# Kernel tuning notes

Measured on AMD Instinct MI355X. Metric: run time of the kernel, lower is better.

Reference implementation:

```python
import jax, jax.numpy as jnp
import numpy as np

N_LAYERS = 2
N_QUBITS = 2


def _ry(t):
    c, s = jnp.cos(t / 2), jnp.sin(t / 2)
    m = jnp.stack([jnp.stack([c, -s], -1), jnp.stack([s, c], -1)], -2)
    return m.astype(jnp.complex64)


def _rx(t):
    c = jnp.cos(t / 2).astype(jnp.complex64)
    s = (-1j) * jnp.sin(t / 2).astype(jnp.complex64)
    return jnp.stack([jnp.stack([c, s], -1), jnp.stack([s, c], -1)], -2)


def _rz(t):
    e = jnp.exp(-0.5j * t.astype(jnp.complex64))
    z = jnp.zeros_like(e)
    return jnp.stack([jnp.stack([e, z], -1), jnp.stack([z, jnp.conj(e)], -1)], -2)


def _apply_w0(G, s):
    # gate on wire 0 (most significant); s: [N,2,2] indexed [n, q0, q1]
    if G.ndim == 2:
        G = G[None]
    return jnp.matmul(G, s)


def _apply_w1(G, s):
    # gate on wire 1: contract last index with G
    if G.ndim == 2:
        G = G[None]
    return jnp.matmul(s, jnp.swapaxes(G, -1, -2))


def _qnn_batched(enc, qw):
    # enc: [N,2] float angles; qw: [2,2,3] trainable angles.
    # Batched 2-qubit statevector simulation, state shape [N,2,2] (q0,q1).
    N = enc.shape[0]
    s = jnp.zeros((N, 2, 2), jnp.complex64).at[:, 0, 0].set(1.0)
    # data encoding: RY(enc_i) on wire i
    s = _apply_w0(_ry(enc[:, 0]), s)
    s = _apply_w1(_ry(enc[:, 1]), s)
    for l in range(N_LAYERS):
        # RX then RY then RZ on each qubit => fused single-qubit gate RZ@RY@RX
        g0 = _rz(qw[l, 0, 2]) @ _ry(qw[l, 0, 1]) @ _rx(qw[l, 0, 0])
        g1 = _rz(qw[l, 1, 2]) @ _ry(qw[l, 1, 1]) @ _rx(qw[l, 1, 0])
        s = _apply_w0(g0, s)
        s = _apply_w1(g1, s)
        # CNOT(control=0, target=1): flip q1 where q0 == 1
        s = s.at[:, 1, :].set(s[:, 1, ::-1])
    p = (s * jnp.conj(s)).real  # probabilities [N,2,2]
    z0 = (p[:, 0, :] - p[:, 1, :]).sum(-1)
    z1 = (p[:, :, 0] - p[:, :, 1]).sum(-1)
    return jnp.stack([z0, z1], -1)  # [N,2]


def _mlp(x, w1, b1, w2, b2, w3, b3):
    h = jnp.tanh(x @ w1 + b1)
    h = jnp.tanh(h @ w2 + b2)
    return h @ w3 + b3


def setup_inputs() -> dict:
    key = jax.random.key(0)
    ks = jax.random.split(key, 15)
    N = 1_000_000
    W = 32

    def rn(k, shape, scale):
        return (scale * jax.random.normal(k, shape)).astype(jnp.float32)

    return {
        "x": rn(ks[0], (N, 1), 1.0),
        "pre_w1": rn(ks[1], (1, W), 1.0),
        "pre_b1": rn(ks[2], (W,), 0.1),
        "pre_w2": rn(ks[3], (W, W), 1.0 / np.sqrt(W)),
        "pre_b2": rn(ks[4], (W,), 0.1),
        "pre_w3": rn(ks[5], (W, 2), 1.0 / np.sqrt(W)),
        "pre_b3": rn(ks[6], (2,), 0.1),
        "q_weights": rn(ks[7], (N_LAYERS, N_QUBITS, 3), 0.1),
        "post_w1": rn(ks[8], (2, W), 1.0 / np.sqrt(2)),
        "post_b1": rn(ks[9], (W,), 0.1),
        "post_w2": rn(ks[10], (W, W), 1.0 / np.sqrt(W)),
        "post_b2": rn(ks[11], (W,), 0.1),
        "post_w3": rn(ks[12], (W, 1), 1.0 / np.sqrt(W)),
        "post_b3": rn(ks[13], (1,), 0.1),
    }


def reference(x, pre_w1, pre_b1, pre_w2, pre_b2, pre_w3, pre_b3, q_weights,
              post_w1, post_b1, post_w2, post_b2, post_w3, post_b3):
    q = _mlp(x, pre_w1, pre_b1, pre_w2, pre_b2, pre_w3, pre_b3)        # [N,2]
    qhat = _qnn_batched(q, q_weights)                                  # [N,2]
    u = _mlp(qhat, post_w1, post_b1, post_w2, post_b2, post_w3, post_b3)  # [N,1]
    return u
```

## Files before the change

### kernel.cpp

```cpp
#include <hip/hip_runtime.h>
#include <hip/hip_bf16.h>
#include <math.h>
#include <stdint.h>


typedef __attribute__((ext_vector_type(8))) short short8;
typedef __attribute__((ext_vector_type(4))) float f32x4;

union Frag { uint32_t u[4]; short8 s; };

#define KT 2.8853900817779268f

#define L_FRAG 0
#define L_U    2048
#define L_W1   2080
#define L_B1   2112
#define L_BH2  2144
#define L_W3   2176
#define L_OW1  2240
#define L_OB1  2304
#define L_BH2P 2336
#define L_OW3  2368
#define L_SC   2400
#define L_TOT  2416

__device__ __forceinline__ float sig_act(float y) {
    return __builtin_amdgcn_rcpf(__builtin_amdgcn_exp2f(y) + 1.0f);
}

__device__ __forceinline__ uint32_t pk_bf16(float a, float b) {
    union { __hip_bfloat162 h; uint32_t u; } cv;
    cv.h.x = __float2bfloat16(a);
    cv.h.y = __float2bfloat16(b);
    return cv.u;
}

__device__ __forceinline__ void split8(const float h[8], uint32_t hi[4], uint32_t lo[4]) {
    #pragma unroll
    for (int p = 0; p < 4; ++p) {
        uint32_t u0 = __float_as_uint(h[2*p])   & 0xFFFF0000u;
        uint32_t u1 = __float_as_uint(h[2*p+1]) & 0xFFFF0000u;
        float l0 = h[2*p]   - __uint_as_float(u0);
        float l1 = h[2*p+1] - __uint_as_float(u1);
        uint32_t v0 = __float_as_uint(l0) & 0xFFFF0000u;
        uint32_t v1 = __float_as_uint(l1) & 0xFFFF0000u;
        hi[p] = (u0 >> 16) | u1;
        lo[p] = (v0 >> 16) | v1;
    }
}

struct cplx { float re, im; };
__device__ __forceinline__ cplx cmul(cplx a, cplx b) {
    return { a.re * b.re - a.im * b.im, a.re * b.im + a.im * b.re };
}
__device__ __forceinline__ cplx cadd(cplx a, cplx b) {
    return { a.re + b.re, a.im + b.im };
}

__global__ void qcpinn_setup(
    const float* __restrict__ pw1, const float* __restrict__ pb1,
    const float* __restrict__ pw2, const float* __restrict__ pb2,
    const float* __restrict__ pw3, const float* __restrict__ pb3,
    const float* __restrict__ qw,
    const float* __restrict__ ow1, const float* __restrict__ ob1,
    const float* __restrict__ ow2, const float* __restrict__ ob2,
    const float* __restrict__ ow3, const float* __restrict__ ob3,
    float* __restrict__ ws)
{
    const int lane = threadIdx.x & 63;
    const int s = lane & 15, gg = lane >> 4;
    uint32_t* wsu = (uint32_t*)ws;

    #pragma unroll
    for (int m = 0; m < 2; ++m) {
        const float* W = m ? ow2 : pw2;
        #pragma unroll
        for (int r = 0; r < 2; ++r) {
            float v[8];
            #pragma unroll
            for (int j = 0; j < 8; ++j)
                v[j] = -2.0f * KT * W[(gg * 8 + j) * 32 + (r * 16 + s)];
            uint32_t hi[4], lo[4];
            split8(v, hi, lo);
            int bh = L_FRAG + ((m * 4 + r * 2 + 0) * 256) + lane * 4;
            int bl = L_FRAG + ((m * 4 + r * 2 + 1) * 256) + lane * 4;
            #pragma unroll
            for (int p = 0; p < 4; ++p) { wsu[bh + p] = hi[p]; wsu[bl + p] = lo[p]; }
        }
    }

    if (lane < 32) {
        int j = lane;
        float cs_p = 0.f, cs_o = 0.f;
        for (int k = 0; k < 32; ++k) { cs_p += pw2[k * 32 + j]; cs_o += ow2[k * 32 + j]; }
        ws[L_W1 + j]   = KT * pw1[j];
        ws[L_B1 + j]   = KT * pb1[j];
        ws[L_BH2 + j]  = KT * (pb2[j] + cs_p);
        ws[L_OB1 + j]  = KT * ob1[j];
        ws[L_BH2P + j] = KT * (ob2[j] + cs_o);
        ws[L_OW3 + j]  = -2.f * ow3[j];
        ws[L_W3 + j * 2]     = -pw3[j * 2];
        ws[L_W3 + j * 2 + 1] = -pw3[j * 2 + 1];
        float sg0 = (j & 16) ? -1.f : 1.f;
        float sg1 = (j & 8)  ? -1.f : 1.f;
        ws[L_OW1 + j]      = KT * sg0 * ow1[j];
        ws[L_OW1 + 32 + j] = KT * sg1 * ow1[32 + j];
    }

    if (lane == 0) {
        float cw0 = 0.f, cw1 = 0.f, co3 = 0.f;
        for (int k = 0; k < 32; ++k) {
            cw0 += pw3[k * 2]; cw1 += pw3[k * 2 + 1]; co3 += ow3[k];
        }
        ws[L_SC + 0] = 0.5f * (pb3[0] + cw0);
        ws[L_SC + 1] = 0.5f * (pb3[1] + cw1);
        ws[L_SC + 2] = ob3[0] + co3;
        ws[L_SC + 3] = 0.f;

        cplx U[16];
        for (int i = 0; i < 16; ++i) U[i] = {0.f, 0.f};
        U[0].re = U[5].re = U[10].re = U[15].re = 1.f;
        for (int l = 0; l < 2; ++l) {
            cplx g[2][4];
            for (int w = 0; w < 2; ++w) {
                float a = qw[l * 6 + w * 3 + 0];
                float b = qw[l * 6 + w * 3 + 1];
                float c = qw[l * 6 + w * 3 + 2];
                float sa, ca, sb, cb, sc, cc;
                __sincosf(0.5f * a, &sa, &ca);
                __sincosf(0.5f * b, &sb, &cb);
                __sincosf(0.5f * c, &sc, &cc);
                cplx RX[4] = {{ca, 0.f}, {0.f, -sa}, {0.f, -sa}, {ca, 0.f}};
                cplx RY[4] = {{cb, 0.f}, {-sb, 0.f}, {sb, 0.f}, {cb, 0.f}};
                cplx RZ[4] = {{cc, -sc}, {0.f, 0.f}, {0.f, 0.f}, {cc, sc}};
                cplx T[4];
                for (int i2 = 0; i2 < 2; ++i2)
                    for (int j2 = 0; j2 < 2; ++j2) {
                        cplx acc = {0.f, 0.f};
                        for (int k2 = 0; k2 < 2; ++k2)
                            acc = cadd(acc, cmul(RY[i2 * 2 + k2], RX[k2 * 2 + j2]));
                        T[i2 * 2 + j2] = acc;
                    }
                for (int i2 = 0; i2 < 2; ++i2)
                    for (int j2 = 0; j2 < 2; ++j2) {
                        cplx acc = {0.f, 0.f};
                        for (int k2 = 0; k2 < 2; ++k2)
                            acc = cadd(acc, cmul(RZ[i2 * 2 + k2], T[k2 * 2 + j2]));
                        g[w][i2 * 2 + j2] = acc;
                    }
            }
            cplx L[16];
            for (int i4 = 0; i4 < 4; ++i4) {
                int si = (i4 == 2) ? 3 : (i4 == 3) ? 2 : i4;
                for (int j4 = 0; j4 < 4; ++j4)
                    L[i4 * 4 + j4] = cmul(g[1][(si & 1) * 2 + (j4 & 1)],
                                          g[0][(si >> 1) * 2 + (j4 >> 1)]);
            }
            cplx Un[16];
            for (int i4 = 0; i4 < 4; ++i4)
                for (int j4 = 0; j4 < 4; ++j4) {
                    cplx acc = {0.f, 0.f};
                    for (int k4 = 0; k4 < 4; ++k4)
                        acc = cadd(acc, cmul(L[i4 * 4 + k4], U[k4 * 4 + j4]));
                    Un[i4 * 4 + j4] = acc;
                }
            for (int i = 0; i < 16; ++i) U[i] = Un[i];
        }
        for (int i = 0; i < 16; ++i) { ws[L_U + i] = U[i].re; ws[L_U + 16 + i] = U[i].im; }
    }
}

#define NT 4
__global__ __launch_bounds__(256) void qcpinn_main(
    const float* __restrict__ x, const float* __restrict__ ws,
    float* __restrict__ out, int N)
{
    __shared__ float lds[L_TOT];
    {
        const float4* src = (const float4*)ws;
        float4* dst = (float4*)lds;
        for (int i = threadIdx.x; i < L_TOT / 4; i += 256) dst[i] = src[i];
    }
    __syncthreads();

    const int lane = threadIdx.x & 63;
    const int wid  = threadIdx.x >> 6;
    const int s    = lane & 15;
    const int g    = lane >> 4;
    const int base = (blockIdx.x * 4 + wid) * 64;

    const Frag* frag = (const Frag*)(lds + L_FRAG);

    float xv[NT];
    #pragma unroll
    for (int t = 0; t < NT; ++t) {
        int idx = base + t * 16 + s;
        xv[t] = (idx < N) ? x[idx] : 0.f;
    }

    f32x4 w1a = *(const f32x4*)(lds + L_W1 + g * 8);
    f32x4 w1b = *(const f32x4*)(lds + L_W1 + g * 8 + 4);
    f32x4 b1a = *(const f32x4*)(lds + L_B1 + g * 8);
    f32x4 b1b = *(const f32x4*)(lds + L_B1 + g * 8 + 4);
    Frag A0h = frag[0 * 64 + lane], A0l = frag[1 * 64 + lane];
    Frag A1h = frag[2 * 64 + lane], A1l = frag[3 * 64 + lane];
    f32x4 bh2a = *(const f32x4*)(lds + L_BH2 + g * 4);
    f32x4 bh2b = *(const f32x4*)(lds + L_BH2 + 16 + g * 4);
    f32x4 w3a = *(const f32x4*)(lds + L_W3 + g * 8);
    f32x4 w3b = *(const f32x4*)(lds + L_W3 + g * 8 + 4);
    f32x4 w3c = *(const f32x4*)(lds + L_W3 + 32 + g * 8);
    f32x4 w3d = *(const f32x4*)(lds + L_W3 + 32 + g * 8 + 4);
    f32x4 Ure = *(const f32x4*)(lds + L_U + g * 4);
    f32x4 Uim = *(const f32x4*)(lds + L_U + 16 + g * 4);
    const float qb0 = lds[L_SC + 0], qb1 = lds[L_SC + 1], bo = lds[L_SC + 2];
    f32x4 oa   = *(const f32x4*)(lds + L_OW1 + g * 8);
    f32x4 oa2  = *(const f32x4*)(lds + L_OW1 + g * 8 + 4);
    f32x4 obv  = *(const f32x4*)(lds + L_OW1 + 32 + g * 8);
    f32x4 ob2v = *(const f32x4*)(lds + L_OW1 + 32 + g * 8 + 4);
    f32x4 obb  = *(const f32x4*)(lds + L_OB1 + g * 8);
    f32x4 obb2 = *(const f32x4*)(lds + L_OB1 + g * 8 + 4);
    Frag P0h = frag[4 * 64 + lane], P0l = frag[5 * 64 + lane];
    Frag P1h = frag[6 * 64 + lane], P1l = frag[7 * 64 + lane];
    f32x4 bpa = *(const f32x4*)(lds + L_BH2P + g * 4);
    f32x4 bpb = *(const f32x4*)(lds + L_BH2P + 16 + g * 4);
    f32x4 w3o0 = *(const f32x4*)(lds + L_OW3 + g * 4);
    f32x4 w3o1 = *(const f32x4*)(lds + L_OW3 + 16 + g * 4);

    float uo[NT];
    #pragma unroll
    for (int t = 0; t < NT; ++t) {
        float r1[8];
        #pragma unroll
        for (int j = 0; j < 4; ++j) {
            r1[j]     = sig_act(fmaf(xv[t], w1a[j], b1a[j]));
            r1[4 + j] = sig_act(fmaf(xv[t], w1b[j], b1b[j]));
        }
        Frag B;
        #pragma unroll
        for (int p = 0; p < 4; ++p) B.u[p] = pk_bf16(r1[2*p], r1[2*p+1]);

        f32x4 C0 = bh2a, C1 = bh2b;
        C0 = __builtin_amdgcn_mfma_f32_16x16x32_bf16(A0h.s, B.s, C0, 0, 0, 0);
        C0 = __builtin_amdgcn_mfma_f32_16x16x32_bf16(A0l.s, B.s, C0, 0, 0, 0);
        C1 = __builtin_amdgcn_mfma_f32_16x16x32_bf16(A1h.s, B.s, C1, 0, 0, 0);
        C1 = __builtin_amdgcn_mfma_f32_16x16x32_bf16(A1l.s, B.s, C1, 0, 0, 0);
        float r2[8];
        #pragma unroll
        for (int i = 0; i < 4; ++i) { r2[i] = sig_act(C0[i]); r2[4+i] = sig_act(C1[i]); }

        float q0, q1;
        q0 = r2[0] * w3a[0];           q1 = r2[0] * w3a[1];
        q0 = fmaf(r2[1], w3a[2], q0);  q1 = fmaf(r2[1], w3a[3], q1);
        q0 = fmaf(r2[2], w3b[0], q0);  q1 = fmaf(r2[2], w3b[1], q1);
        q0 = fmaf(r2[3], w3b[2], q0);  q1 = fmaf(r2[3], w3b[3], q1);
        q0 = fmaf(r2[4], w3c[0], q0);  q1 = fmaf(r2[4], w3c[1], q1);
        q0 = fmaf(r2[5], w3c[2], q0);  q1 = fmaf(r2[5], w3c[3], q1);
        q0 = fmaf(r2[6], w3d[0], q0);  q1 = fmaf(r2[6], w3d[1], q1);
        q0 = fmaf(r2[7], w3d[2], q0);  q1 = fmaf(r2[7], w3d[3], q1);
        q0 += __shfl_xor(q0, 16); q0 += __shfl_xor(q0, 32); q0 += qb0;
        q1 += __shfl_xor(q1, 16); q1 += __shfl_xor(q1, 32); q1 += qb1;

        float s0, c0, s1, c1;
        __sincosf(q0, &s0, &c0);
        __sincosf(q1, &s1, &c1);
        float e0 = c0 * c1, e1 = c0 * s1, e2 = s0 * c1, e3 = s0 * s1;
        float re = fmaf(Ure[0], e0, fmaf(Ure[1], e1, fmaf(Ure[2], e2, Ure[3] * e3)));
        float im = fmaf(Uim[0], e0, fmaf(Uim[1], e1, fmaf(Uim[2], e2, Uim[3] * e3)));
        float p  = fmaf(re, re, im * im);

        float pr   = __shfl_xor(p, 16);
        float sm   = p + pr, df = p - pr;
        float z0pm = sm - __shfl_xor(sm, 32);
        float z1pm = df + __shfl_xor(df, 32);

        float r3[8];
        #pragma unroll
        for (int j = 0; j < 4; ++j) {
            r3[j]     = sig_act(fmaf(z0pm, oa[j],  fmaf(z1pm, obv[j],  obb[j])));
            r3[4 + j] = sig_act(fmaf(z0pm, oa2[j], fmaf(z1pm, ob2v[j], obb2[j])));
        }
        Frag B2;
        #pragma unroll
        for (int p2 = 0; p2 < 4; ++p2) B2.u[p2] = pk_bf16(r3[2*p2], r3[2*p2+1]);

        f32x4 D0 = bpa, D1 = bpb;
        D0 = __builtin_amdgcn_mfma_f32_16x16x32_bf16(P0h.s, B2.s, D0, 0, 0, 0);
        D0 = __builtin_amdgcn_mfma_f32_16x16x32_bf16(P0l.s, B2.s, D0, 0, 0, 0);
        D1 = __builtin_amdgcn_mfma_f32_16x16x32_bf16(P1h.s, B2.s, D1, 0, 0, 0);
        D1 = __builtin_amdgcn_mfma_f32_16x16x32_bf16(P1l.s, B2.s, D1, 0, 0, 0);

        float u = 0.f;
        #pragma unroll
        for (int i = 0; i < 4; ++i) {
            u = fmaf(sig_act(D0[i]), w3o0[i], u);
            u = fmaf(sig_act(D1[i]), w3o1[i], u);
        }
        u += __shfl_xor(u, 16);
        u += __shfl_xor(u, 32);
        uo[t] = u;
    }

    float ua = (g & 1) ? uo[1] : uo[0];
    float ub = (g & 1) ? uo[3] : uo[2];
    float us = ((g & 2) ? ub : ua) + bo;
    int oidx = base + lane;
    if (oidx < N) out[oidx] = us;
}

extern "C" void kernel_launch(void* const* d_in, const int* in_sizes, int n_in,
                              void* d_out, int out_size, void* d_ws, size_t ws_size,
                              hipStream_t stream) {
    const float* x   = (const float*)d_in[0];
    const float* pw1 = (const float*)d_in[1];
    const float* pb1 = (const float*)d_in[2];
    const float* pw2 = (const float*)d_in[3];
    const float* pb2 = (const float*)d_in[4];
    const float* pw3 = (const float*)d_in[5];
    const float* pb3 = (const float*)d_in[6];
    const float* qw  = (const float*)d_in[7];
    const float* ow1 = (const float*)d_in[8];
    const float* ob1 = (const float*)d_in[9];
    const float* ow2 = (const float*)d_in[10];
    const float* ob2 = (const float*)d_in[11];
    const float* ow3 = (const float*)d_in[12];
    const float* ob3 = (const float*)d_in[13];
    float* out = (float*)d_out;
    float* ws  = (float*)d_ws;

    const int N = in_sizes[0];

    qcpinn_setup<<<1, 64, 0, stream>>>(pw1, pb1, pw2, pb2, pw3, pb3, qw,
                                       ow1, ob1, ow2, ob2, ow3, ob3, ws);

    const int grid = (N + 255) / 256;
    qcpinn_main<<<grid, 256, 0, stream>>>(x, ws, out, N);
}
```

Before: 118.8 us.

## Process two sample tiles per iteration with packed float2 math

Doubles the samples per wave (NT 4→8) and handles two 16-sample tiles per loop iteration, using two-wide float vectors so the compiler can emit packed FMA/mul and interleave two independent MFMA chains. The grid is halved accordingly and each thread writes two outputs. The setup kernel also splits the column-sum loops across all 64 lanes. This raises instruction-level parallelism and amortizes per-wave LDS parameter loads, at the cost of higher register pressure and fewer waves.

```diff
diff --git a/kernel.cpp b/kernel.cpp
--- a/kernel.cpp
+++ b/kernel.cpp
@@ -6,6 +6,7 @@
 
 typedef __attribute__((ext_vector_type(8))) short short8;
 typedef __attribute__((ext_vector_type(4))) float f32x4;
+typedef __attribute__((ext_vector_type(2))) float f32x2;
 
 union Frag { uint32_t u[4]; short8 s; };
 
@@ -24,10 +25,23 @@
 #define L_SC   2400
 #define L_TOT  2416
 
-__device__ __forceinline__ float sig_act(float y) {
-    return __builtin_amdgcn_rcpf(__builtin_amdgcn_exp2f(y) + 1.0f);
-}
-
+__device__ __forceinline__ f32x2 splat2(float v) { return (f32x2){v, v}; }
+__device__ __forceinline__ f32x2 fma2(f32x2 a, f32x2 b, f32x2 c) {
+    return __builtin_elementwise_fma(a, b, c);
+}
+__device__ __forceinline__ f32x2 sig2(f32x2 y) {
+    f32x2 e;
+    e.x = __builtin_amdgcn_exp2f(y.x);
+    e.y = __builtin_amdgcn_exp2f(y.y);
+    e = e + 1.0f;
+    f32x2 r;
+    r.x = __builtin_amdgcn_rcpf(e.x);
+    r.y = __builtin_amdgcn_rcpf(e.y);
+    return r;
+}
+__device__ __forceinline__ f32x2 shfl2(f32x2 v, int m) {
+    f32x2 r; r.x = __shfl_xor(v.x, m); r.y = __shfl_xor(v.y, m); return r;
+}
 __device__ __forceinline__ uint32_t pk_bf16(float a, float b) {
     union { __hip_bfloat162 h; uint32_t u; } cv;
     cv.h.x = __float2bfloat16(a);
@@ -89,16 +103,21 @@
         }
     }
 
+    {
+        int j = lane & 31;
+        const float* W = (lane < 32) ? pw2 : ow2;
+        float cs = 0.f;
+        for (int k = 0; k < 32; ++k) cs += W[k * 32 + j];
+        if (lane < 32) ws[L_BH2  + j] = KT * (pb2[j] + cs);
+        else           ws[L_BH2P + j] = KT * (ob2[j] + cs);
+    }
+
     if (lane < 32) {
         int j = lane;
-        float cs_p = 0.f, cs_o = 0.f;
-        for (int k = 0; k < 32; ++k) { cs_p += pw2[k * 32 + j]; cs_o += ow2[k * 32 + j]; }
-        ws[L_W1 + j]   = KT * pw1[j];
-        ws[L_B1 + j]   = KT * pb1[j];
-        ws[L_BH2 + j]  = KT * (pb2[j] + cs_p);
-        ws[L_OB1 + j]  = KT * ob1[j];
-        ws[L_BH2P + j] = KT * (ob2[j] + cs_o);
-        ws[L_OW3 + j]  = -2.f * ow3[j];
+        ws[L_W1 + j]  = KT * pw1[j];
+        ws[L_B1 + j]  = KT * pb1[j];
+        ws[L_OB1 + j] = KT * ob1[j];
+        ws[L_OW3 + j] = -2.f * ow3[j];
         ws[L_W3 + j * 2]     = -pw3[j * 2];
         ws[L_W3 + j * 2 + 1] = -pw3[j * 2 + 1];
         float sg0 = (j & 16) ? -1.f : 1.f;
@@ -170,7 +189,7 @@
     }
 }
 
-#define NT 4
+#define NT 8
 __global__ __launch_bounds__(256) void qcpinn_main(
     const float* __restrict__ x, const float* __restrict__ ws,
     float* __restrict__ out, int N)
@@ -187,7 +206,7 @@
     const int wid  = threadIdx.x >> 6;
     const int s    = lane & 15;
     const int g    = lane >> 4;
-    const int base = (blockIdx.x * 4 + wid) * 64;
+    const int base = (blockIdx.x * 4 + wid) * (NT * 16);
 
     const Frag* frag = (const Frag*)(lds + L_FRAG);
 
@@ -228,83 +247,114 @@
 
     float uo[NT];
     #pragma unroll
-    for (int t = 0; t < NT; ++t) {
-        float r1[8];
+    for (int p = 0; p < NT / 2; ++p) {
+        f32x2 xv2 = (f32x2){xv[2 * p], xv[2 * p + 1]};
+
+        f32x2 r1v[8];
         #pragma unroll
         for (int j = 0; j < 4; ++j) {
-            r1[j]     = sig_act(fmaf(xv[t], w1a[j], b1a[j]));
-            r1[4 + j] = sig_act(fmaf(xv[t], w1b[j], b1b[j]));
-        }
-        Frag B;
-        #pragma unroll
-        for (int p = 0; p < 4; ++p) B.u[p] = pk_bf16(r1[2*p], r1[2*p+1]);
-
-        f32x4 C0 = bh2a, C1 = bh2b;
-        C0 = __builtin_amdgcn_mfma_f32_16x16x32_bf16(A0h.s, B.s, C0, 0, 0, 0);
-        C0 = __builtin_amdgcn_mfma_f32_16x16x32_bf16(A0l.s, B.s, C0, 0, 0, 0);
-        C1 = __builtin_amdgcn_mfma_f32_16x16x32_bf16(A1h.s, B.s, C1, 0, 0, 0);
-        C1 = __builtin_amdgcn_mfma_f32_16x16x32_bf16(A1l.s, B.s, C1, 0, 0, 0);
-        float r2[8];
-        #pragma unroll
-        for (int i = 0; i < 4; ++i) { r2[i] = sig_act(C0[i]); r2[4+i] = sig_act(C1[i]); }
-
-        float q0, q1;
-        q0 = r2[0] * w3a[0];           q1 = r2[0] * w3a[1];
-        q0 = fmaf(r2[1], w3a[2], q0);  q1 = fmaf(r2[1], w3a[3], q1);
-        q0 = fmaf(r2[2], w3b[0], q0);  q1 = fmaf(r2[2], w3b[1], q1);
-        q0 = fmaf(r2[3], w3b[2], q0);  q1 = fmaf(r2[3], w3b[3], q1);
-        q0 = fmaf(r2[4], w3c[0], q0);  q1 = fmaf(r2[4], w3c[1], q1);
-        q0 = fmaf(r2[5], w3c[2], q0);  q1 = fmaf(r2[5], w3c[3], q1);
-        q0 = fmaf(r2[6], w3d[0], q0);  q1 = fmaf(r2[6], w3d[1], q1);
-        q0 = fmaf(r2[7], w3d[2], q0);  q1 = fmaf(r2[7], w3d[3], q1);
-        q0 += __shfl_xor(q0, 16); q0 += __shfl_xor(q0, 32); q0 += qb0;
-        q1 += __shfl_xor(q1, 16); q1 += __shfl_xor(q1, 32); q1 += qb1;
-
-        float s0, c0, s1, c1;
-        __sincosf(q0, &s0, &c0);
-        __sincosf(q1, &s1, &c1);
-        float e0 = c0 * c1, e1 = c0 * s1, e2 = s0 * c1, e3 = s0 * s1;
-        float re = fmaf(Ure[0], e0, fmaf(Ure[1], e1, fmaf(Ure[2], e2, Ure[3] * e3)));
-        float im = fmaf(Uim[0], e0, fmaf(Uim[1], e1, fmaf(Uim[2], e2, Uim[3] * e3)));
-        float p  = fmaf(re, re, im * im);
-
-        float pr   = __shfl_xor(p, 16);
-        float sm   = p + pr, df = p - pr;
-        float z0pm = sm - __shfl_xor(sm, 32);
-        float z1pm = df + __shfl_xor(df, 32);
-
-        float r3[8];
+            r1v[j]     = sig2(fma2(xv2, splat2(w1a[j]), splat2(b1a[j])));
+            r1v[4 + j] = sig2(fma2(xv2, splat2(w1b[j]), splat2(b1b[j])));
+        }
+        Frag Be, Bo;
+        #pragma unroll
+        for (int w = 0; w < 4; ++w) {
+            Be.u[w] = pk_bf16(r1v[2 * w].x, r1v[2 * w + 1].x);
+            Bo.u[w] = pk_bf16(r1v[2 * w].y, r1v[2 * w + 1].y);
+        }
+
+        f32x4 C0e = bh2a, C1e = bh2b, C0o = bh2a, C1o = bh2b;
+        C0e = __builtin_amdgcn_mfma_f32_16x16x32_bf16(A0h.s, Be.s, C0e, 0, 0, 0);
+        C0e = __builtin_amdgcn_mfma_f32_16x16x32_bf16(A0l.s, Be.s, C0e, 0, 0, 0);
+        C1e = __builtin_amdgcn_mfma_f32_16x16x32_bf16(A1h.s, Be.s, C1e, 0, 0, 0);
+        C1e = __builtin_amdgcn_mfma_f32_16x16x32_bf16(A1l.s, Be.s, C1e, 0, 0, 0);
+        C0o = __builtin_amdgcn_mfma_f32_16x16x32_bf16(A0h.s, Bo.s, C0o, 0, 0, 0);
+        C0o = __builtin_amdgcn_mfma_f32_16x16x32_bf16(A0l.s, Bo.s, C0o, 0, 0, 0);
+        C1o = __builtin_amdgcn_mfma_f32_16x16x32_bf16(A1h.s, Bo.s, C1o, 0, 0, 0);
+        C1o = __builtin_amdgcn_mfma_f32_16x16x32_bf16(A1l.s, Bo.s, C1o, 0, 0, 0);
+
+        f32x2 r2v[8];
+        #pragma unroll
+        for (int i = 0; i < 4; ++i) {
+            r2v[i]     = sig2((f32x2){C0e[i], C0o[i]});
+            r2v[4 + i] = sig2((f32x2){C1e[i], C1o[i]});
+        }
+
+        f32x2 q0 = r2v[0] * splat2(w3a[0]);
+        f32x2 q1 = r2v[0] * splat2(w3a[1]);
+        q0 = fma2(r2v[1], splat2(w3a[2]), q0); q1 = fma2(r2v[1], splat2(w3a[3]), q1);
+        q0 = fma2(r2v[2], splat2(w3b[0]), q0); q1 = fma2(r2v[2], splat2(w3b[1]), q1);
+        q0 = fma2(r2v[3], splat2(w3b[2]), q0); q1 = fma2(r2v[3], splat2(w3b[3]), q1);
+        q0 = fma2(r2v[4], splat2(w3c[0]), q0); q1 = fma2(r2v[4], splat2(w3c[1]), q1);
+        q0 = fma2(r2v[5], splat2(w3c[2]), q0); q1 = fma2(r2v[5], splat2(w3c[3]), q1);
+        q0 = fma2(r2v[6], splat2(w3d[0]), q0); q1 = fma2(r2v[6], splat2(w3d[1]), q1);
+        q0 = fma2(r2v[7], splat2(w3d[2]), q0); q1 = fma2(r2v[7], splat2(w3d[3]), q1);
+        q0 += shfl2(q0, 16); q0 += shfl2(q0, 32); q0 += splat2(qb0);
+        q1 += shfl2(q1, 16); q1 += shfl2(q1, 32); q1 += splat2(qb1);
+
+        float s0x, c0x, s0y, c0y, s1x, c1x, s1y, c1y;
+        __sincosf(q0.x, &s0x, &c0x); __sincosf(q0.y, &s0y, &c0y);
+        __sincosf(q1.x, &s1x, &c1x); __sincosf(q1.y, &s1y, &c1y);
+        f32x2 s0 = (f32x2){s0x, s0y}, c0 = (f32x2){c0x, c0y};
+        f32x2 s1 = (f32x2){s1x, s1y}, c1 = (f32x2){c1x, c1y};
+        f32x2 e0 = c0 * c1, e1 = c0 * s1, e2 = s0 * c1, e3 = s0 * s1;
+        f32x2 re = fma2(splat2(Ure[0]), e0, fma2(splat2(Ure[1]), e1,
+                   fma2(splat2(Ure[2]), e2, splat2(Ure[3]) * e3)));
+        f32x2 im = fma2(splat2(Uim[0]), e0, fma2(splat2(Uim[1]), e1,
+                   fma2(splat2(Uim[2]), e2, splat2(Uim[3]) * e3)));
+        f32x2 pq = fma2(re, re, im * im);
+
+        f32x2 pr = shfl2(pq, 16);
+        f32x2 sm = pq + pr, df = pq - pr;
+        f32x2 z0 = sm - shfl2(sm, 32);
+        f32x2 z1 = df + shfl2(df, 32);
+
+        f32x2 r3v[8];
         #pragma unroll
         for (int j = 0; j < 4; ++j) {
-            r3[j]     = sig_act(fmaf(z0pm, oa[j],  fmaf(z1pm, obv[j],  obb[j])));
-            r3[4 + j] = sig_act(fmaf(z0pm, oa2[j], fmaf(z1pm, ob2v[j], obb2[j])));
-        }
-        Frag B2;
-        #pragma unroll
-        for (int p2 = 0; p2 < 4; ++p2) B2.u[p2] = pk_bf16(r3[2*p2], r3[2*p2+1]);
-
-        f32x4 D0 = bpa, D1 = bpb;
-        D0 = __builtin_amdgcn_mfma_f32_16x16x32_bf16(P0h.s, B2.s, D0, 0, 0, 0);
-        D0 = __builtin_amdgcn_mfma_f32_16x16x32_bf16(P0l.s, B2.s, D0, 0, 0, 0);
-        D1 = __builtin_amdgcn_mfma_f32_16x16x32_bf16(P1h.s, B2.s, D1, 0, 0, 0);
-        D1 = __builtin_amdgcn_mfma_f32_16x16x32_bf16(P1l.s, B2.s, D1, 0, 0, 0);
-
-        float u = 0.f;
+            r3v[j]     = sig2(fma2(z0, splat2(oa[j]),
+                              fma2(z1, splat2(obv[j]),  splat2(obb[j]))));
+            r3v[4 + j] = sig2(fma2(z0, splat2(oa2[j]),
+                              fma2(z1, splat2(ob2v[j]), splat2(obb2[j]))));
+        }
+        Frag B2e, B2o;
+        #pragma unroll
+        for (int w = 0; w < 4; ++w) {
+            B2e.u[w] = pk_bf16(r3v[2 * w].x, r3v[2 * w + 1].x);
+            B2o.u[w] = pk_bf16(r3v[2 * w].y, r3v[2 * w + 1].y);
+        }
+
+        f32x4 D0e = bpa, D1e = bpb, D0o = bpa, D1o = bpb;
+        D0e = __builtin_amdgcn_mfma_f32_16x16x32_bf16(P0h.s, B2e.s, D0e, 0, 0, 0);
+        D0e = __builtin_amdgcn_mfma_f32_16x16x32_bf16(P0l.s, B2e.s, D0e, 0, 0, 0);
+        D1e = __builtin_amdgcn_mfma_f32_16x16x32_bf16(P1h.s, B2e.s, D1e, 0, 0, 0);
+        D1e = __builtin_amdgcn_mfma_f32_16x16x32_bf16(P1l.s, B2e.s, D1e, 0, 0, 0);
+        D0o = __builtin_amdgcn_mfma_f32_16x16x32_bf16(P0h.s, B2o.s, D0o, 0, 0, 0);
+        D0o = __builtin_amdgcn_mfma_f32_16x16x32_bf16(P0l.s, B2o.s, D0o, 0, 0, 0);
+        D1o = __builtin_amdgcn_mfma_f32_16x16x32_bf16(P1h.s, B2o.s, D1o, 0, 0, 0);
+        D1o = __builtin_amdgcn_mfma_f32_16x16x32_bf16(P1l.s, B2o.s, D1o, 0, 0, 0);
+
+        f32x2 u = splat2(0.f);
         #pragma unroll
         for (int i = 0; i < 4; ++i) {
-            u = fmaf(sig_act(D0[i]), w3o0[i], u);
-            u = fmaf(sig_act(D1[i]), w3o1[i], u);
-        }
-        u += __shfl_xor(u, 16);
-        u += __shfl_xor(u, 32);
-        uo[t] = u;
+            u = fma2(sig2((f32x2){D0e[i], D0o[i]}), splat2(w3o0[i]), u);
+            u = fma2(sig2((f32x2){D1e[i], D1o[i]}), splat2(w3o1[i]), u);
+        }
+        u += shfl2(u, 16);
+        u += shfl2(u, 32);
+        uo[2 * p]     = u.x;
+        uo[2 * p + 1] = u.y;
     }
 
     float ua = (g & 1) ? uo[1] : uo[0];
     float ub = (g & 1) ? uo[3] : uo[2];
-    float us = ((g & 2) ? ub : ua) + bo;
-    int oidx = base + lane;
-    if (oidx < N) out[oidx] = us;
+    float us0 = ((g & 2) ? ub : ua) + bo;
+    float uc = (g & 1) ? uo[5] : uo[4];
+    float ud = (g & 1) ? uo[7] : uo[6];
+    float us1 = ((g & 2) ? ud : uc) + bo;
+    int o0 = base + lane, o1 = base + 64 + lane;
+    if (o0 < N) out[o0] = us0;
+    if (o1 < N) out[o1] = us1;
 }
 
 extern "C" void kernel_launch(void* const* d_in, const int* in_sizes, int n_in,
@@ -332,6 +382,6 @@
     qcpinn_setup<<<1, 64, 0, stream>>>(pw1, pb1, pw2, pb2, pw3, pb3, qw,
                                        ow1, ob1, ow2, ob2, ow3, ob3, ws);
 
-    const int grid = (N + 255) / 256;
+    const int grid = (N + 511) / 512;
     qcpinn_main<<<grid, 256, 0, stream>>>(x, ws, out, N);
 }
```

Measured after the change: 117.5 us. About the same (-1.1%).
